# Kernel optimization log

Measured on AMD Instinct MI355X. Metric: run time of the kernel, lower is better.

Reference implementation:

```python
import jax, jax.numpy as jnp
import numpy as np

B, L, D, H = 2, 2048, 512, 8
SAMPLING_FACTOR = 5


def setup_inputs() -> dict:
    key = jax.random.key(0)
    ks = jax.random.split(key, 12)
    L_K = min(8000, L)
    log_L_K = int(np.ceil(np.log1p(L_K)))
    U_part = min(SAMPLING_FACTOR * L * log_L_K, L_K)  # = 2048
    inp = {
        'q': jax.random.normal(ks[0], (B, L, D), jnp.float32),
        'k': jax.random.normal(ks[1], (B, L, D), jnp.float32),
        'v': jax.random.normal(ks[2], (B, L, D), jnp.float32),
        'Wq': jax.random.normal(ks[3], (D, D), jnp.float32) * 0.02,
        'bq': jnp.zeros((D,), jnp.float32),
        'Wk': jax.random.normal(ks[4], (D, D), jnp.float32) * 0.02,
        'bk': jnp.zeros((D,), jnp.float32),
        'Wv': jax.random.normal(ks[5], (D, D), jnp.float32) * 0.02,
        'bv': jnp.zeros((D,), jnp.float32),
        'Wo': jax.random.normal(ks[6], (D, D), jnp.float32) * 0.02,
        'bo': jnp.zeros((D,), jnp.float32),
        'index_sample': jax.random.randint(ks[7], (U_part,), 0, L_K, jnp.int32),
    }
    return inp


def _prob_sparse(qh, Kh, Vh, index_sample):
    # qh, Kh, Vh: [B, H, L, d]
    L_K = min(8000, Kh.shape[2])  # K_sample = K[:, :8000]; L_K = its length
    L_Q = qh.shape[2]
    Ks = Kh[:, :, index_sample, :]                                  # [B,H,U,d]
    QKs = jnp.einsum('bhqd,bhkd->bhqk', qh, Ks)                     # [B,H,Lq,U]
    # M = max - sum/L_K  (source divides by L_K, not U_part)
    M = QKs.max(axis=-1) - QKs.sum(axis=-1) / L_K                   # [B,H,Lq]
    u = min(SAMPLING_FACTOR * int(np.ceil(np.log1p(L_Q))), L_Q)     # = 40
    _, M_top = jax.lax.top_k(-M, u)                                 # topk(largest=False)
    Q_red = jnp.take_along_axis(qh, M_top[..., None], axis=2)       # [B,H,u,d]
    d_k = qh.shape[-1]
    scores = jnp.einsum('bhqd,bhkd->bhqk', Q_red, Kh) / jnp.sqrt(jnp.asarray(d_k, qh.dtype))
    probs = jax.nn.softmax(scores, axis=-1)
    out = jnp.einsum('bhqk,bhkd->bhqd', probs, Vh)                  # [B,H,u,d]
    return out, scores


def reference(q, k, v, Wq, bq, Wk, bk, Wv, bv, Wo, bo, index_sample):
    qp = q @ Wq.T + bq
    kp = k @ Wk.T + bk
    vp = v @ Wv.T + bv
    Bsz, Lq, Dm = qp.shape
    d = Dm // H
    # faithful to source: q is view'd to [B,H,Lq,d] WITHOUT transpose
    qh = qp.reshape(Bsz, H, Lq, d)
    kh = kp.reshape(Bsz, -1, H, d).transpose(0, 2, 1, 3)
    vh = vp.reshape(Bsz, -1, H, d).transpose(0, 2, 1, 3)
    out, _ = _prob_sparse(qh, kh, vh, index_sample)
    u = out.shape[2]
    out = out.transpose(0, 2, 1, 3).reshape(Bsz, u, Dm)             # concat
    return out @ Wo.T + bo                                          # [B,u,D]
```

## Files before the change

### kernel.cpp

```cpp
#include <hip/hip_runtime.h>
#include <math.h>

#define B_ 2
#define L_ 2048
#define D_ 512
#define H_ 8
#define DH 64
#define NS 2048
#define NU 40
#define BHD (L_*D_)
#define QHS (L_*DH)
#define WSPM 786432

typedef __attribute__((ext_vector_type(8))) short bf16x8;
typedef __attribute__((ext_vector_type(4))) float f32x4;

__device__ inline float4 ld4(const float* p) { return *reinterpret_cast<const float4*>(p); }

__device__ inline unsigned short hi16(float x) { return (unsigned short)(__float_as_uint(x) >> 16); }
__device__ inline float trunchf(float x) { return __uint_as_float(__float_as_uint(x) & 0xFFFF0000u); }
__device__ inline void tsplit(float x, unsigned short& hs, unsigned short& ms, unsigned short& ls) {
  float h = trunchf(x); hs = hi16(x);
  float r = x - h;
  float m = trunchf(r); ms = hi16(r);
  float r2 = r - m;
  ls = hi16(r2);
}

__global__ __launch_bounds__(256) void wsplit(const float* __restrict__ Wq,
                                              const float* __restrict__ Wk,
                                              const float* __restrict__ Wv,
                                              unsigned short* __restrict__ dst,
                                              int matArg) {
  const int mat = (matArg >= 0) ? matArg : (int)blockIdx.y;
  const float* W = (mat == 0) ? Wq : (mat == 1) ? Wk : Wv;
  unsigned short* d = dst + ((matArg >= 0) ? 0 : (size_t)mat * WSPM);
  const int t = threadIdx.x;
  const int nt = blockIdx.x >> 3, g16 = blockIdx.x & 7;
  const int kc = t >> 4, lr = t & 15;
  const int n = nt*128 + g16*16 + lr;
  const float* src = W + (size_t)n*512 + kc*32;
  float xs[32];
#pragma unroll
  for (int i = 0; i < 8; ++i) {
    float4 v4 = ld4(src + 4*i);
    xs[4*i] = v4.x; xs[4*i+1] = v4.y; xs[4*i+2] = v4.z; xs[4*i+3] = v4.w;
  }
  unsigned short Hs[32], Ms[32], Ls[32];
#pragma unroll
  for (int e = 0; e < 32; ++e) tsplit(xs[e], Hs[e], Ms[e], Ls[e]);
#pragma unroll
  for (int p = 0; p < 3; ++p) {
    const unsigned short* sp = (p == 0) ? Hs : (p == 1) ? Ms : Ls;
    unsigned short* base = d + ((size_t)((p*4 + nt)*8 + g16)*16 + kc)*512;
#pragma unroll
    for (int lg = 0; lg < 4; ++lg) {
      union { bf16x8 v; unsigned short u[8]; } P;
#pragma unroll
      for (int e = 0; e < 8; ++e) P.u[e] = sp[lg*8 + e];
      *reinterpret_cast<bf16x8*>(base + (lr + 16*lg)*8) = P.v;
    }
  }
}

__global__ __launch_bounds__(256, 2) void proj_pipe(
    const float* __restrict__ qa, const float* __restrict__ ka, const float* __restrict__ va,
    const unsigned short* __restrict__ wsp,
    const float* __restrict__ bq, const float* __restrict__ bk, const float* __restrict__ bv,
    float* __restrict__ qp, float* __restrict__ kp, float* __restrict__ vp,
    int matArg)
{
  __shared__ __align__(16) unsigned short a3[2][3][128][36];
  const int t = threadIdx.x;
  const int mat = (matArg >= 0) ? matArg : (int)blockIdx.z;
  const float* A    = (mat == 0) ? qa : (mat == 1) ? ka : va;
  const float* bias = (mat == 0) ? bq : (mat == 1) ? bk : bv;
  float* C          = (mat == 0) ? qp : (mat == 1) ? kp : vp;
  const unsigned short* wspm = wsp + ((matArg >= 0) ? 0 : (size_t)mat * WSPM);
  const int m0 = blockIdx.x * 128, nt = blockIdx.y;
  const int w = t >> 6, l = t & 63;
  const int wm = w >> 1, wn = w & 1;
  const int lr = l & 15, lg = l >> 4;
  const int srow = t >> 1, sc0 = (t & 1) * 16;

  f32x4 acc[4][4];
#pragma unroll
  for (int i = 0; i < 4; ++i)
#pragma unroll
    for (int j = 0; j < 4; ++j) acc[i][j] = (f32x4){0.f, 0.f, 0.f, 0.f};

  const float* aRow = A + (size_t)(m0 + srow) * 512 + sc0;
  float4 ar0 = ld4(aRow), ar1 = ld4(aRow + 4), ar2 = ld4(aRow + 8), ar3 = ld4(aRow + 12);

  for (int kc = 0; kc < 16; ++kc) {
    const int cur = kc & 1;
    {
      float xs[16] = {ar0.x, ar0.y, ar0.z, ar0.w, ar1.x, ar1.y, ar1.z, ar1.w,
                      ar2.x, ar2.y, ar2.z, ar2.w, ar3.x, ar3.y, ar3.z, ar3.w};
#pragma unroll
      for (int hh = 0; hh < 2; ++hh) {
        union { bf16x8 v; unsigned short u[8]; } H, M, L;
#pragma unroll
        for (int e = 0; e < 8; ++e) tsplit(xs[hh*8 + e], H.u[e], M.u[e], L.u[e]);
        *reinterpret_cast<bf16x8*>(&a3[cur][0][srow][sc0 + 8*hh]) = H.v;
        *reinterpret_cast<bf16x8*>(&a3[cur][1][srow][sc0 + 8*hh]) = M.v;
        *reinterpret_cast<bf16x8*>(&a3[cur][2][srow][sc0 + 8*hh]) = L.v;
      }
    }
    bf16x8 bw[3][4];
#pragma unroll
    for (int p = 0; p < 3; ++p)
#pragma unroll
      for (int ni = 0; ni < 4; ++ni)
        bw[p][ni] = *reinterpret_cast<const bf16x8*>(
            wspm + ((size_t)((p*4 + nt)*8 + wn*4 + ni)*16 + kc)*512 + l*8);
    __syncthreads();
    if (kc < 15) {
      const float* src = A + (size_t)(m0 + srow) * 512 + (kc+1)*32 + sc0;
      ar0 = ld4(src); ar1 = ld4(src + 4); ar2 = ld4(src + 8); ar3 = ld4(src + 12);
    }
    __builtin_amdgcn_s_setprio(1);
#pragma unroll
    for (int mi = 0; mi < 4; ++mi) {
      bf16x8 a0 = *reinterpret_cast<const bf16x8*>(&a3[cur][0][wm*64 + mi*16 + lr][lg*8]);
      bf16x8 a1 = *reinterpret_cast<const bf16x8*>(&a3[cur][1][wm*64 + mi*16 + lr][lg*8]);
      bf16x8 a2 = *reinterpret_cast<const bf16x8*>(&a3[cur][2][wm*64 + mi*16 + lr][lg*8]);
#pragma unroll
      for (int ni = 0; ni < 4; ++ni) {
        acc[mi][ni] = __builtin_amdgcn_mfma_f32_16x16x32_bf16(a0, bw[0][ni], acc[mi][ni], 0, 0, 0);
        acc[mi][ni] = __builtin_amdgcn_mfma_f32_16x16x32_bf16(a0, bw[1][ni], acc[mi][ni], 0, 0, 0);
        acc[mi][ni] = __builtin_amdgcn_mfma_f32_16x16x32_bf16(a1, bw[0][ni], acc[mi][ni], 0, 0, 0);
        acc[mi][ni] = __builtin_amdgcn_mfma_f32_16x16x32_bf16(a1, bw[1][ni], acc[mi][ni], 0, 0, 0);
        acc[mi][ni] = __builtin_amdgcn_mfma_f32_16x16x32_bf16(a0, bw[2][ni], acc[mi][ni], 0, 0, 0);
        acc[mi][ni] = __builtin_amdgcn_mfma_f32_16x16x32_bf16(a2, bw[0][ni], acc[mi][ni], 0, 0, 0);
      }
    }
    __builtin_amdgcn_s_setprio(0);
  }
#pragma unroll
  for (int mi = 0; mi < 4; ++mi)
#pragma unroll
    for (int ni = 0; ni < 4; ++ni) {
      const int gn = nt*128 + wn*64 + ni*16 + lr;
      const float bv_ = bias[gn];
#pragma unroll
      for (int r = 0; r < 4; ++r) {
        const int gm = m0 + wm*64 + mi*16 + lg*4 + r;
        C[(size_t)gm * 512 + gn] = acc[mi][ni][r] + bv_;
      }
    }
}

__global__ __launch_bounds__(1024) void ksum_kernel(const float* __restrict__ kp,
                                                    const int* __restrict__ idx,
                                                    float* __restrict__ ksum) {
  __shared__ float part[16][64];
  const int bh = blockIdx.x;
  const int b = bh >> 3, h = bh & 7;
  const int t = threadIdx.x;
  const int sg = t >> 6, j = t & 63;
  const float* kbase = kp + (size_t)b*BHD + h*DH;
  float a = 0.f;
  for (int s = sg*128; s < sg*128 + 128; ++s)
    a += kbase[(size_t)idx[s]*512 + j];
  part[sg][j] = a;
  __syncthreads();
  if (t < 64) {
    float s = 0.f;
#pragma unroll
    for (int i = 0; i < 16; ++i) s += part[i][t];
    ksum[bh*64 + t] = s;
  }
}

__global__ __launch_bounds__(256, 2) void m_kernel(const float* __restrict__ qp,
                                                   const float* __restrict__ kp,
                                                   const int* __restrict__ idx,
                                                   float* __restrict__ Mp) {
  __shared__ __align__(16) unsigned short k3[3][128][72];
  const int t = threadIdx.x;
  const int bid = blockIdx.x;
  const int bh = bid >> 5, qt = (bid >> 2) & 7, ks = bid & 3;
  const int b = bh >> 3, h = bh & 7;
  const int w = t >> 6, l = t & 63;
  const int lr = l & 15;
  const int lg = l >> 4;

  bf16x8 qf[4][2][3];
  {
    const float* qbase = qp + (size_t)b*BHD + (size_t)h*QHS + (size_t)(qt*256 + w*64 + lr) * 64 + lg*8;
#pragma unroll
    for (int mi = 0; mi < 4; ++mi)
#pragma unroll
      for (int c = 0; c < 2; ++c) {
        const float* src = qbase + mi*16*64 + c*32;
        float4 x0 = ld4(src), x1 = ld4(src + 4);
        float xs[8] = {x0.x, x0.y, x0.z, x0.w, x1.x, x1.y, x1.z, x1.w};
        union { bf16x8 v; unsigned short u[8]; } H, M, L;
#pragma unroll
        for (int e = 0; e < 8; ++e) tsplit(xs[e], H.u[e], M.u[e], L.u[e]);
        qf[mi][c][0] = H.v; qf[mi][c][1] = M.v; qf[mi][c][2] = L.v;
      }
  }

  const float* kbase = kp + (size_t)b*BHD + h*DH;
  const int ib = ks * 512;
  const int srow = t >> 1, sh = (t & 1) * 32;

  float4 vst[8];
  {
    const int kr = idx[ib + srow];
    const float* src = kbase + (size_t)kr * 512 + sh;
#pragma unroll
    for (int i = 0; i < 8; ++i) vst[i] = ld4(src + 4*i);
  }

  float mx[4][4];
#pragma unroll
  for (int mi = 0; mi < 4; ++mi)
#pragma unroll
    for (int r = 0; r < 4; ++r) mx[mi][r] = -INFINITY;

  for (int tl = 0; tl < 4; ++tl) {
    __syncthreads();
    {
#pragma unroll
      for (int e2 = 0; e2 < 4; ++e2) {
        union { bf16x8 v; unsigned short u[8]; } H, M, L;
        float xs[8] = {vst[2*e2].x, vst[2*e2].y, vst[2*e2].z, vst[2*e2].w,
                       vst[2*e2+1].x, vst[2*e2+1].y, vst[2*e2+1].z, vst[2*e2+1].w};
#pragma unroll
        for (int e = 0; e < 8; ++e) tsplit(xs[e], H.u[e], M.u[e], L.u[e]);
        *reinterpret_cast<bf16x8*>(&k3[0][srow][sh + 8*e2]) = H.v;
        *reinterpret_cast<bf16x8*>(&k3[1][srow][sh + 8*e2]) = M.v;
        *reinterpret_cast<bf16x8*>(&k3[2][srow][sh + 8*e2]) = L.v;
      }
    }
    if (tl < 3) {
      const int kr = idx[ib + (tl+1)*128 + srow];
      const float* src = kbase + (size_t)kr * 512 + sh;
#pragma unroll
      for (int i = 0; i < 8; ++i) vst[i] = ld4(src + 4*i);
    }
    __syncthreads();

    for (int n2 = 0; n2 < 4; ++n2) {
      bf16x8 bf[2][3][2];
#pragma unroll
      for (int ns = 0; ns < 2; ++ns)
#pragma unroll
        for (int p = 0; p < 3; ++p)
#pragma unroll
          for (int c = 0; c < 2; ++c)
            bf[ns][p][c] = *reinterpret_cast<const bf16x8*>(&k3[p][n2*32 + ns*16 + lr][c*32 + lg*8]);
      __builtin_amdgcn_s_setprio(1);
#pragma unroll
      for (int mi = 0; mi < 4; ++mi)
#pragma unroll
        for (int ns = 0; ns < 2; ++ns) {
          f32x4 acc = {0.f, 0.f, 0.f, 0.f};
#pragma unroll
          for (int c = 0; c < 2; ++c) acc = __builtin_amdgcn_mfma_f32_16x16x32_bf16(qf[mi][c][0], bf[ns][0][c], acc, 0, 0, 0);
#pragma unroll
          for (int c = 0; c < 2; ++c) acc = __builtin_amdgcn_mfma_f32_16x16x32_bf16(qf[mi][c][0], bf[ns][1][c], acc, 0, 0, 0);
#pragma unroll
          for (int c = 0; c < 2; ++c) acc = __builtin_amdgcn_mfma_f32_16x16x32_bf16(qf[mi][c][1], bf[ns][0][c], acc, 0, 0, 0);
#pragma unroll
          for (int c = 0; c < 2; ++c) acc = __builtin_amdgcn_mfma_f32_16x16x32_bf16(qf[mi][c][1], bf[ns][1][c], acc, 0, 0, 0);
#pragma unroll
          for (int c = 0; c < 2; ++c) acc = __builtin_amdgcn_mfma_f32_16x16x32_bf16(qf[mi][c][0], bf[ns][2][c], acc, 0, 0, 0);
#pragma unroll
          for (int c = 0; c < 2; ++c) acc = __builtin_amdgcn_mfma_f32_16x16x32_bf16(qf[mi][c][2], bf[ns][0][c], acc, 0, 0, 0);
#pragma unroll
          for (int r = 0; r < 4; ++r) mx[mi][r] = fmaxf(mx[mi][r], acc[r]);
        }
      __builtin_amdgcn_s_setprio(0);
    }
  }

#pragma unroll
  for (int mi = 0; mi < 4; ++mi)
#pragma unroll
    for (int r = 0; r < 4; ++r) {
      float v = mx[mi][r];
      v = fmaxf(v, __shfl_xor(v, 1));
      v = fmaxf(v, __shfl_xor(v, 2));
      v = fmaxf(v, __shfl_xor(v, 4));
      v = fmaxf(v, __shfl_xor(v, 8));
      if (lr == 0)
        Mp[ks*32768 + bh*2048 + qt*256 + w*64 + mi*16 + lg*4 + r] = v;
    }
}

__global__ __launch_bounds__(256) void topk_kernel(const float* __restrict__ qp,
                                                   const float* __restrict__ ksum,
                                                   const float* __restrict__ Mp,
                                                   int* __restrict__ Mtop) {
  __shared__ float ks_s[64];
  __shared__ unsigned hist[256];
  __shared__ int wsum[4];
  __shared__ unsigned bitmap[64];
  __shared__ unsigned long long comb[NU];
  __shared__ int s_sel, s_rem, s_cnt;
  const int bh = blockIdx.x;
  const int b = bh >> 3, h = bh & 7;
  const int t = threadIdx.x;
  if (t < 64) ks_s[t] = ksum[bh*64 + t];
  __syncthreads();

  unsigned mykey[8];
#pragma unroll
  for (int c = 0; c < 8; ++c) {
    const int qi = c * 256 + t;
    const float* qrow = qp + (size_t)b*BHD + (size_t)h*QHS + (size_t)qi * 64;
    float dot = 0.f;
#pragma unroll
    for (int cc = 0; cc < 16; ++cc) {
      float4 q4 = ld4(qrow + 4 * cc);
      dot += q4.x * ks_s[4*cc + 0];
      dot += q4.y * ks_s[4*cc + 1];
      dot += q4.z * ks_s[4*cc + 2];
      dot += q4.w * ks_s[4*cc + 3];
    }
    const float mx2 = fmaxf(fmaxf(Mp[bh*2048 + qi], Mp[32768 + bh*2048 + qi]),
                            fmaxf(Mp[65536 + bh*2048 + qi], Mp[98304 + bh*2048 + qi]));
    const float m = mx2 - dot * (1.0f/2048.0f);
    const unsigned u = __float_as_uint(m);
    mykey[c] = (u >> 31) ? ~u : (u | 0x80000000u);
  }

  unsigned prefMask = 0u, prefVal = 0u;
  int rem = NU;
  for (int shift = 24; shift >= 0; shift -= 8) {
    hist[t] = 0;
    __syncthreads();
#pragma unroll
    for (int c = 0; c < 8; ++c) {
      const unsigned key = mykey[c];
      if ((key & prefMask) == prefVal)
        atomicAdd(&hist[(key >> shift) & 255], 1u);
    }
    __syncthreads();
    const int binc = (int)hist[t];
    int inc = binc;
#pragma unroll
    for (int off = 1; off < 64; off <<= 1) {
      const int nb = __shfl_up(inc, off);
      if ((t & 63) >= off) inc += nb;
    }
    if ((t & 63) == 63) wsum[t >> 6] = inc;
    __syncthreads();
    int wadd = 0;
    for (int w2 = 0; w2 < (t >> 6); ++w2) wadd += wsum[w2];
    const int incl = inc + wadd;
    const int excl = incl - binc;
    if (excl < rem && rem <= incl) { s_sel = t; s_rem = rem - excl; }
    __syncthreads();
    prefVal |= ((unsigned)s_sel) << shift;
    prefMask |= 0xFFu << shift;
    rem = s_rem;
    __syncthreads();
  }
  const unsigned T = prefVal;

  if (t < 64) bitmap[t] = 0;
  if (t == 0) s_cnt = 0;
  __syncthreads();
#pragma unroll
  for (int c = 0; c < 8; ++c) {
    const unsigned key = mykey[c];
    const int qi = c * 256 + t;
    if (key < T) {
      const int pos = atomicAdd(&s_cnt, 1);
      comb[pos] = ((unsigned long long)key << 11) | (unsigned)qi;
    } else if (key == T) {
      atomicOr(&bitmap[qi >> 5], 1u << (qi & 31));
    }
  }
  __syncthreads();
  if (t == 0) {
    int need = rem, cpos = s_cnt;
    for (int wd = 0; wd < 64 && need > 0; ++wd) {
      unsigned bits = bitmap[wd];
      while (bits && need > 0) {
        const int bit = __ffs(bits) - 1;
        bits &= bits - 1;
        comb[cpos++] = ((unsigned long long)T << 11) | (unsigned)(wd*32 + bit);
        --need;
      }
    }
  }
  __syncthreads();

  if (t < 64) {
    const unsigned long long mine = (t < NU) ? comb[t] : ~0ULL;
    int rank = 0;
#pragma unroll
    for (int step = 1; step < 64; ++step) {
      const unsigned long long other = __shfl(mine, (t + step) & 63);
      rank += (other < mine) ? 1 : 0;
    }
    if (t < NU) Mtop[bh*NU + rank] = (int)(mine & 0x7FFu);
  }
}

__global__ __launch_bounds__(256) void flash_partial(const float* __restrict__ qp,
                                                     const float* __restrict__ kp,
                                                     const float* __restrict__ vp,
                                                     const int* __restrict__ Mtop,
                                                     float* __restrict__ pm,
                                                     float* __restrict__ pl,
                                                     float* __restrict__ pacc) {
  __shared__ float qr[NU][65];
  __shared__ float kv[64][65];
  __shared__ float sl[NU][65];
  __shared__ float ms[NU], ls[NU], fs[NU];
  const int bid = blockIdx.x;
  const int bh = bid >> 4, kt = bid & 15;
  const int b = bh >> 3, h = bh & 7;
  const int t = threadIdx.x;
  const int g = t >> 6, j = t & 63;
  const int r4 = t >> 2, sub = t & 3;

  {
    const float* qbase = qp + (size_t)b*BHD + (size_t)h*QHS;
#pragma unroll
    for (int r = 0; r < 10; ++r) {
      const int q = g*10 + r;
      qr[q][j] = qbase[(size_t)Mtop[bh*NU + q]*64 + j];
    }
  }
  if (t < NU) { ms[t] = -INFINITY; ls[t] = 0.f; }
  float acc[10];
#pragma unroll
  for (int r = 0; r < 10; ++r) acc[r] = 0.f;

  const float* kbase = kp + (size_t)b*BHD + h*DH;
  const float* vbase = vp + (size_t)b*BHD + h*DH;
  const int srow = t >> 2, scb = (t & 3)*16;

  for (int st = 0; st < 2; ++st) {
    const int kb = kt*128 + st*64;
    __syncthreads();
    {
      const float* src = kbase + (size_t)(kb + srow)*512 + scb;
#pragma unroll
      for (int i = 0; i < 4; ++i) {
        float4 v = ld4(src + 4*i);
        kv[srow][scb + 4*i + 0] = v.x;
        kv[srow][scb + 4*i + 1] = v.y;
        kv[srow][scb + 4*i + 2] = v.z;
        kv[srow][scb + 4*i + 3] = v.w;
      }
    }
    __syncthreads();
    {
      float sv[10];
#pragma unroll
      for (int r = 0; r < 10; ++r) {
        const int q = g*10 + r;
        float s = 0.f;
#pragma unroll 8
        for (int jj = 0; jj < 64; ++jj) s += qr[q][jj]*kv[j][jj];
        sv[r] = s * 0.125f;
      }
#pragma unroll
      for (int r = 0; r < 10; ++r) sl[g*10 + r][j] = sv[r];
    }
    __syncthreads();
    float4 vst[4];
    {
      const float* src = vbase + (size_t)(kb + srow)*512 + scb;
#pragma unroll
      for (int i = 0; i < 4; ++i) vst[i] = ld4(src + 4*i);
    }
    if (r4 < NU) {
      float tm = -INFINITY;
#pragma unroll
      for (int c = 0; c < 16; ++c) tm = fmaxf(tm, sl[r4][sub*16 + c]);
      tm = fmaxf(tm, __shfl_xor(tm, 1));
      tm = fmaxf(tm, __shfl_xor(tm, 2));
      const float nm = fmaxf(ms[r4], tm);
      if (sub == 0) { fs[r4] = expf(ms[r4] - nm); ms[r4] = nm; }
    }
    __syncthreads();
    {
#pragma unroll
      for (int r = 0; r < 10; ++r) {
        const int q = g*10 + r;
        acc[r] *= fs[q];
        sl[q][j] = expf(sl[q][j] - ms[q]);
      }
#pragma unroll
      for (int i = 0; i < 4; ++i) {
        kv[srow][scb + 4*i + 0] = vst[i].x;
        kv[srow][scb + 4*i + 1] = vst[i].y;
        kv[srow][scb + 4*i + 2] = vst[i].z;
        kv[srow][scb + 4*i + 3] = vst[i].w;
      }
    }
    __syncthreads();
    if (r4 < NU) {
      float s = 0.f;
#pragma unroll
      for (int c = 0; c < 16; ++c) s += sl[r4][sub*16 + c];
      s += __shfl_xor(s, 1);
      s += __shfl_xor(s, 2);
      if (sub == 0) ls[r4] = ls[r4]*fs[r4] + s;
    }
    {
#pragma unroll 4
      for (int kk = 0; kk < 64; ++kk) {
        const float vv = kv[kk][j];
#pragma unroll
        for (int r = 0; r < 10; ++r) acc[r] += sl[g*10 + r][kk]*vv;
      }
    }
  }
  __syncthreads();
  const size_t base = (size_t)(bh*16 + kt)*NU;
  if (t < NU) { pm[base + t] = ms[t]; pl[base + t] = ls[t]; }
#pragma unroll
  for (int r = 0; r < 10; ++r)
    pacc[(base + g*10 + r)*64 + j] = acc[r];
}

__global__ __launch_bounds__(256) void flash_combine(const float* __restrict__ pm,
                                                     const float* __restrict__ pl,
                                                     const float* __restrict__ pacc,
                                                     float* __restrict__ outc) {
  const int t = threadIdx.x;
  const int qg = t >> 6, j = t & 63;
  const int bh = blockIdx.x / 10;
  const int q  = (blockIdx.x % 10)*4 + qg;
  const int b = bh >> 3, h = bh & 7;
  float m = -INFINITY;
#pragma unroll
  for (int kt = 0; kt < 16; ++kt) m = fmaxf(m, pm[(size_t)(bh*16 + kt)*NU + q]);
  float Lsum = 0.f, num = 0.f;
#pragma unroll
  for (int kt = 0; kt < 16; ++kt) {
    const size_t base = (size_t)(bh*16 + kt)*NU;
    const float w = expf(pm[base + q] - m);
    Lsum += w * pl[base + q];
    num  += w * pacc[(base + q)*64 + j];
  }
  outc[(size_t)(b*NU + q)*512 + h*64 + j] = num / Lsum;
}

__global__ __launch_bounds__(256) void wo_gemm(const float* __restrict__ outc,
                                               const float* __restrict__ Wo,
                                               float* __restrict__ pwo) {
  __shared__ __align__(16) float a_t[80][68];
  __shared__ __align__(16) float w_t[64][68];
  const int t = threadIdx.x;
  const int ty = t >> 4, tx = t & 15;
  const int nt = blockIdx.x, ks = blockIdx.y;
  float acc[5][4];
#pragma unroll
  for (int i = 0; i < 5; ++i)
#pragma unroll
    for (int j = 0; j < 4; ++j) acc[i][j] = 0.f;

  for (int c = 0; c < 2; ++c) {
    const int kb = ks*128 + c*64;
    __syncthreads();
#pragma unroll
    for (int i = 0; i < 20; ++i) {
      const int fi = t + 256*i;
      const int row = fi >> 6, col = fi & 63;
      a_t[row][col] = outc[(size_t)row*512 + kb + col];
    }
#pragma unroll
    for (int i = 0; i < 16; ++i) {
      const int fi = t + 256*i;
      const int row = fi >> 6, col = fi & 63;
      w_t[row][col] = Wo[(size_t)(nt*64 + row)*512 + kb + col];
    }
    __syncthreads();
    for (int gq = 0; gq < 16; ++gq) {
      float4 av[5], wv[4];
#pragma unroll
      for (int i = 0; i < 5; ++i) av[i] = *reinterpret_cast<const float4*>(&a_t[ty + 16*i][4*gq]);
#pragma unroll
      for (int j = 0; j < 4; ++j) wv[j] = *reinterpret_cast<const float4*>(&w_t[tx + 16*j][4*gq]);
#pragma unroll
      for (int i = 0; i < 5; ++i)
#pragma unroll
        for (int j = 0; j < 4; ++j) {
          acc[i][j] += av[i].x * wv[j].x;
          acc[i][j] += av[i].y * wv[j].y;
          acc[i][j] += av[i].z * wv[j].z;
          acc[i][j] += av[i].w * wv[j].w;
        }
    }
  }
#pragma unroll
  for (int i = 0; i < 5; ++i)
#pragma unroll
    for (int j = 0; j < 4; ++j)
      pwo[ks*40960 + (size_t)(ty + 16*i)*512 + nt*64 + tx + 16*j] = acc[i][j];
}

__global__ __launch_bounds__(256) void wo_combine(const float* __restrict__ pwo,
                                                  const float* __restrict__ bo,
                                                  float* __restrict__ out) {
  const int gi = blockIdx.x*256 + threadIdx.x;
  const float4* p = reinterpret_cast<const float4*>(pwo);
  const float4 a = p[gi], b4 = p[10240 + gi], c4 = p[20480 + gi], d4 = p[30720 + gi];
  const float4 bb = ld4(bo + 4*(gi & 127));
  float4 o;
  o.x = a.x + b4.x + c4.x + d4.x + bb.x;
  o.y = a.y + b4.y + c4.y + d4.y + bb.y;
  o.z = a.z + b4.z + c4.z + d4.z + bb.z;
  o.w = a.w + b4.w + c4.w + d4.w + bb.w;
  reinterpret_cast<float4*>(out)[gi] = o;
}

extern "C" void kernel_launch(void* const* d_in, const int* in_sizes, int n_in,
                              void* d_out, int out_size, void* d_ws, size_t ws_size,
                              hipStream_t stream) {
  const float* q  = (const float*)d_in[0];
  const float* k  = (const float*)d_in[1];
  const float* v  = (const float*)d_in[2];
  const float* Wq = (const float*)d_in[3];
  const float* bq = (const float*)d_in[4];
  const float* Wk = (const float*)d_in[5];
  const float* bk = (const float*)d_in[6];
  const float* Wv = (const float*)d_in[7];
  const float* bv = (const float*)d_in[8];
  const float* Wo = (const float*)d_in[9];
  const float* bo = (const float*)d_in[10];
  const int*  idx = (const int*)d_in[11];

  float* ws   = (float*)d_ws;
  float* qp   = ws;
  float* kp   = ws + 2097152;
  float* vp   = ws + 4194304;
  float* ksum = ws + 6291456;
  int*   Mtop = (int*)(ws + 6292480);
  float* pm   = ws + 6293120;
  float* pl   = ws + 6303360;
  float* pacc = ws + 6313600;
  float* outc = ws + 6968960;
  float* Mp   = pm;
  float* pwo  = pm;
  unsigned short* wsp = (unsigned short*)(ws + 6291456);

  const dim3 blk(256);
  const bool bigws = (ws_size >= (size_t)7471104 * 4);
  if (bigws) {
    wsplit<<<dim3(32, 3), blk, 0, stream>>>(Wq, Wk, Wv, wsp, -1);
    proj_pipe<<<dim3(32, 4, 3), blk, 0, stream>>>(q, k, v, wsp, bq, bk, bv, qp, kp, vp, -1);
  } else {
    for (int m = 0; m < 3; ++m) {
      wsplit<<<dim3(32, 1), blk, 0, stream>>>(Wq, Wk, Wv, wsp, m);
      proj_pipe<<<dim3(32, 4, 1), blk, 0, stream>>>(q, k, v, wsp, bq, bk, bv, qp, kp, vp, m);
    }
  }
  ksum_kernel<<<dim3(16), dim3(1024), 0, stream>>>(kp, idx, ksum);
  m_kernel<<<dim3(512), blk, 0, stream>>>(qp, kp, idx, Mp);
  topk_kernel<<<dim3(16), blk, 0, stream>>>(qp, ksum, Mp, Mtop);
  flash_partial<<<dim3(256), blk, 0, stream>>>(qp, kp, vp, Mtop, pm, pl, pacc);
  flash_combine<<<dim3(160), blk, 0, stream>>>(pm, pl, pacc, outc);
  wo_gemm<<<dim3(8, 4), blk, 0, stream>>>(outc, Wo, pwo);
  wo_combine<<<dim3(40), blk, 0, stream>>>(pwo, bo, (float*)d_out);
}
```

Measured before the change: 189.8 us.

## Deduplicate sampled key indices for the max pass and double-buffer projection weights

A new single-block kernel builds a bitmap of the sampled key indices and compacts it into a sorted unique list, padded to whole 128-row tiles. The max-score kernel then loops only over the unique tiles, since duplicates cannot change a max, and splits the key range 8 ways instead of 4 to keep the larger grid busy. The row sum still uses the full index list, so duplicates are still counted there. Separately, the projection GEMM is unrolled by two with ping-pong registers so the next step's weight fragments and input rows are prefetched before the current MFMA block runs. Costs: an extra launch, a serial single-block dedupe, more partial-max buffers for top-k to read, and higher register pressure in the projection.

```diff
diff --git a/kernel.cpp b/kernel.cpp
--- a/kernel.cpp
+++ b/kernel.cpp
@@ -82,6 +82,7 @@
   const int wm = w >> 1, wn = w & 1;
   const int lr = l & 15, lg = l >> 4;
   const int srow = t >> 1, sc0 = (t & 1) * 16;
+  const float* aRow = A + (size_t)(m0 + srow) * 512 + sc0;
 
   f32x4 acc[4][4];
 #pragma unroll
@@ -89,54 +90,75 @@
 #pragma unroll
     for (int j = 0; j < 4; ++j) acc[i][j] = (f32x4){0.f, 0.f, 0.f, 0.f};
 
-  const float* aRow = A + (size_t)(m0 + srow) * 512 + sc0;
-  float4 ar0 = ld4(aRow), ar1 = ld4(aRow + 4), ar2 = ld4(aRow + 8), ar3 = ld4(aRow + 12);
-
-  for (int kc = 0; kc < 16; ++kc) {
-    const int cur = kc & 1;
-    {
-      float xs[16] = {ar0.x, ar0.y, ar0.z, ar0.w, ar1.x, ar1.y, ar1.z, ar1.w,
-                      ar2.x, ar2.y, ar2.z, ar2.w, ar3.x, ar3.y, ar3.z, ar3.w};
-#pragma unroll
-      for (int hh = 0; hh < 2; ++hh) {
-        union { bf16x8 v; unsigned short u[8]; } H, M, L;
-#pragma unroll
-        for (int e = 0; e < 8; ++e) tsplit(xs[hh*8 + e], H.u[e], M.u[e], L.u[e]);
-        *reinterpret_cast<bf16x8*>(&a3[cur][0][srow][sc0 + 8*hh]) = H.v;
-        *reinterpret_cast<bf16x8*>(&a3[cur][1][srow][sc0 + 8*hh]) = M.v;
-        *reinterpret_cast<bf16x8*>(&a3[cur][2][srow][sc0 + 8*hh]) = L.v;
-      }
-    }
-    bf16x8 bw[3][4];
-#pragma unroll
-    for (int p = 0; p < 3; ++p)
-#pragma unroll
-      for (int ni = 0; ni < 4; ++ni)
-        bw[p][ni] = *reinterpret_cast<const bf16x8*>(
-            wspm + ((size_t)((p*4 + nt)*8 + wn*4 + ni)*16 + kc)*512 + l*8);
+#define LOADW(dst, kcv)                                                        \
+  _Pragma("unroll")                                                            \
+  for (int p = 0; p < 3; ++p)                                                  \
+    _Pragma("unroll")                                                          \
+    for (int ni = 0; ni < 4; ++ni)                                             \
+      dst[p][ni] = *reinterpret_cast<const bf16x8*>(                           \
+          wspm + ((size_t)((p*4 + nt)*8 + wn*4 + ni)*16 + (kcv))*512 + l*8);
+
+#define SPLITSTORE(r0, r1, r2, r3, buf)                                        \
+  {                                                                            \
+    float xs[16] = {r0.x, r0.y, r0.z, r0.w, r1.x, r1.y, r1.z, r1.w,            \
+                    r2.x, r2.y, r2.z, r2.w, r3.x, r3.y, r3.z, r3.w};           \
+    _Pragma("unroll")                                                          \
+    for (int hh = 0; hh < 2; ++hh) {                                           \
+      union { bf16x8 v; unsigned short u[8]; } H, M, L;                        \
+      _Pragma("unroll")                                                        \
+      for (int e = 0; e < 8; ++e) tsplit(xs[hh*8 + e], H.u[e], M.u[e], L.u[e]);\
+      *reinterpret_cast<bf16x8*>(&a3[buf][0][srow][sc0 + 8*hh]) = H.v;         \
+      *reinterpret_cast<bf16x8*>(&a3[buf][1][srow][sc0 + 8*hh]) = M.v;         \
+      *reinterpret_cast<bf16x8*>(&a3[buf][2][srow][sc0 + 8*hh]) = L.v;         \
+    }                                                                          \
+  }
+
+#define MFMA6(buf, bw)                                                         \
+  __builtin_amdgcn_s_setprio(1);                                               \
+  _Pragma("unroll")                                                            \
+  for (int mi = 0; mi < 4; ++mi) {                                             \
+    bf16x8 a0 = *reinterpret_cast<const bf16x8*>(&a3[buf][0][wm*64 + mi*16 + lr][lg*8]); \
+    bf16x8 a1 = *reinterpret_cast<const bf16x8*>(&a3[buf][1][wm*64 + mi*16 + lr][lg*8]); \
+    bf16x8 a2 = *reinterpret_cast<const bf16x8*>(&a3[buf][2][wm*64 + mi*16 + lr][lg*8]); \
+    _Pragma("unroll")                                                          \
+    for (int ni = 0; ni < 4; ++ni) {                                           \
+      acc[mi][ni] = __builtin_amdgcn_mfma_f32_16x16x32_bf16(a0, bw[0][ni], acc[mi][ni], 0, 0, 0); \
+      acc[mi][ni] = __builtin_amdgcn_mfma_f32_16x16x32_bf16(a0, bw[1][ni], acc[mi][ni], 0, 0, 0); \
+      acc[mi][ni] = __builtin_amdgcn_mfma_f32_16x16x32_bf16(a1, bw[0][ni], acc[mi][ni], 0, 0, 0); \
+      acc[mi][ni] = __builtin_amdgcn_mfma_f32_16x16x32_bf16(a1, bw[1][ni], acc[mi][ni], 0, 0, 0); \
+      acc[mi][ni] = __builtin_amdgcn_mfma_f32_16x16x32_bf16(a0, bw[2][ni], acc[mi][ni], 0, 0, 0); \
+      acc[mi][ni] = __builtin_amdgcn_mfma_f32_16x16x32_bf16(a2, bw[0][ni], acc[mi][ni], 0, 0, 0); \
+    }                                                                          \
+  }                                                                            \
+  __builtin_amdgcn_s_setprio(0);
+
+  float4 arA0 = ld4(aRow), arA1 = ld4(aRow + 4), arA2 = ld4(aRow + 8), arA3 = ld4(aRow + 12);
+  bf16x8 bwA[3][4], bwB[3][4];
+  LOADW(bwA, 0);
+  float4 arB0, arB1, arB2, arB3;
+
+  for (int kc = 0; kc < 16; kc += 2) {
+    SPLITSTORE(arA0, arA1, arA2, arA3, 0);
     __syncthreads();
     if (kc < 15) {
-      const float* src = A + (size_t)(m0 + srow) * 512 + (kc+1)*32 + sc0;
-      ar0 = ld4(src); ar1 = ld4(src + 4); ar2 = ld4(src + 8); ar3 = ld4(src + 12);
-    }
-    __builtin_amdgcn_s_setprio(1);
-#pragma unroll
-    for (int mi = 0; mi < 4; ++mi) {
-      bf16x8 a0 = *reinterpret_cast<const bf16x8*>(&a3[cur][0][wm*64 + mi*16 + lr][lg*8]);
-      bf16x8 a1 = *reinterpret_cast<const bf16x8*>(&a3[cur][1][wm*64 + mi*16 + lr][lg*8]);
-      bf16x8 a2 = *reinterpret_cast<const bf16x8*>(&a3[cur][2][wm*64 + mi*16 + lr][lg*8]);
-#pragma unroll
-      for (int ni = 0; ni < 4; ++ni) {
-        acc[mi][ni] = __builtin_amdgcn_mfma_f32_16x16x32_bf16(a0, bw[0][ni], acc[mi][ni], 0, 0, 0);
-        acc[mi][ni] = __builtin_amdgcn_mfma_f32_16x16x32_bf16(a0, bw[1][ni], acc[mi][ni], 0, 0, 0);
-        acc[mi][ni] = __builtin_amdgcn_mfma_f32_16x16x32_bf16(a1, bw[0][ni], acc[mi][ni], 0, 0, 0);
-        acc[mi][ni] = __builtin_amdgcn_mfma_f32_16x16x32_bf16(a1, bw[1][ni], acc[mi][ni], 0, 0, 0);
-        acc[mi][ni] = __builtin_amdgcn_mfma_f32_16x16x32_bf16(a0, bw[2][ni], acc[mi][ni], 0, 0, 0);
-        acc[mi][ni] = __builtin_amdgcn_mfma_f32_16x16x32_bf16(a2, bw[0][ni], acc[mi][ni], 0, 0, 0);
-      }
-    }
-    __builtin_amdgcn_s_setprio(0);
-  }
+      const float* src = aRow + (kc+1)*32;
+      arB0 = ld4(src); arB1 = ld4(src + 4); arB2 = ld4(src + 8); arB3 = ld4(src + 12);
+      LOADW(bwB, kc+1);
+    }
+    MFMA6(0, bwA);
+    SPLITSTORE(arB0, arB1, arB2, arB3, 1);
+    __syncthreads();
+    if (kc + 2 < 16) {
+      const float* src = aRow + (kc+2)*32;
+      arA0 = ld4(src); arA1 = ld4(src + 4); arA2 = ld4(src + 8); arA3 = ld4(src + 12);
+      LOADW(bwA, kc+2);
+    }
+    MFMA6(1, bwB);
+  }
+#undef LOADW
+#undef SPLITSTORE
+#undef MFMA6
+
 #pragma unroll
   for (int mi = 0; mi < 4; ++mi)
 #pragma unroll
@@ -173,14 +195,60 @@
   }
 }
 
+__global__ __launch_bounds__(256) void dedupe(const int* __restrict__ idx,
+                                              int* __restrict__ ulist,
+                                              int* __restrict__ ucnt) {
+  __shared__ unsigned bm[64];
+  __shared__ int base[64];
+  __shared__ int total;
+  const int t = threadIdx.x;
+  if (t < 64) bm[t] = 0;
+  __syncthreads();
+#pragma unroll
+  for (int c = 0; c < 8; ++c) {
+    const int v = idx[c*256 + t];
+    atomicOr(&bm[v >> 5], 1u << (v & 31));
+  }
+  __syncthreads();
+  if (t < 64) {
+    const int cnt = __popc(bm[t]);
+    int inc = cnt;
+#pragma unroll
+    for (int off = 1; off < 64; off <<= 1) {
+      const int nb = __shfl_up(inc, off);
+      if (t >= off) inc += nb;
+    }
+    base[t] = inc - cnt;
+    if (t == 63) total = inc;
+  }
+  __syncthreads();
+  if (t < 64) {
+    unsigned w = bm[t];
+    int pos = base[t];
+    while (w) {
+      const int b = __ffs(w) - 1;
+      w &= w - 1;
+      ulist[pos++] = t*32 + b;
+    }
+  }
+  __syncthreads();
+  const int U = total;
+  const int nt = (U + 127) >> 7;
+  const int padded = nt << 7;
+  const int first = ulist[0];
+  for (int p = U + t; p < padded; p += 256) ulist[p] = first;
+  if (t == 0) ucnt[0] = nt;
+}
+
 __global__ __launch_bounds__(256, 2) void m_kernel(const float* __restrict__ qp,
                                                    const float* __restrict__ kp,
-                                                   const int* __restrict__ idx,
+                                                   const int* __restrict__ ulist,
+                                                   const int* __restrict__ ucnt,
                                                    float* __restrict__ Mp) {
   __shared__ __align__(16) unsigned short k3[3][128][72];
   const int t = threadIdx.x;
   const int bid = blockIdx.x;
-  const int bh = bid >> 5, qt = (bid >> 2) & 7, ks = bid & 3;
+  const int bh = bid >> 6, qt = (bid >> 3) & 7, ks = bid & 7;
   const int b = bh >> 3, h = bh & 7;
   const int w = t >> 6, l = t & 63;
   const int lr = l & 15;
@@ -204,12 +272,12 @@
   }
 
   const float* kbase = kp + (size_t)b*BHD + h*DH;
-  const int ib = ks * 512;
+  const int ntiles = ucnt[0];
   const int srow = t >> 1, sh = (t & 1) * 32;
 
   float4 vst[8];
-  {
-    const int kr = idx[ib + srow];
+  if (ks < ntiles) {
+    const int kr = ulist[ks*128 + srow];
     const float* src = kbase + (size_t)kr * 512 + sh;
 #pragma unroll
     for (int i = 0; i < 8; ++i) vst[i] = ld4(src + 4*i);
@@ -221,7 +289,7 @@
 #pragma unroll
     for (int r = 0; r < 4; ++r) mx[mi][r] = -INFINITY;
 
-  for (int tl = 0; tl < 4; ++tl) {
+  for (int ti = ks; ti < ntiles; ti += 8) {
     __syncthreads();
     {
 #pragma unroll
@@ -236,8 +304,8 @@
         *reinterpret_cast<bf16x8*>(&k3[2][srow][sh + 8*e2]) = L.v;
       }
     }
-    if (tl < 3) {
-      const int kr = idx[ib + (tl+1)*128 + srow];
+    if (ti + 8 < ntiles) {
+      const int kr = ulist[(ti+8)*128 + srow];
       const float* src = kbase + (size_t)kr * 512 + sh;
 #pragma unroll
       for (int i = 0; i < 8; ++i) vst[i] = ld4(src + 4*i);
@@ -322,9 +390,10 @@
       dot += q4.z * ks_s[4*cc + 2];
       dot += q4.w * ks_s[4*cc + 3];
     }
-    const float mx2 = fmaxf(fmaxf(Mp[bh*2048 + qi], Mp[32768 + bh*2048 + qi]),
-                            fmaxf(Mp[65536 + bh*2048 + qi], Mp[98304 + bh*2048 + qi]));
-    const float m = mx2 - dot * (1.0f/2048.0f);
+    float mxv = Mp[bh*2048 + qi];
+#pragma unroll
+    for (int s = 1; s < 8; ++s) mxv = fmaxf(mxv, Mp[s*32768 + bh*2048 + qi]);
+    const float m = mxv - dot * (1.0f/2048.0f);
     const unsigned u = __float_as_uint(m);
     mykey[c] = (u >> 31) ? ~u : (u | 0x80000000u);
   }
@@ -646,6 +715,8 @@
   float* Mp   = pm;
   float* pwo  = pm;
   unsigned short* wsp = (unsigned short*)(ws + 6291456);
+  int* ulist = (int*)(ws + 6600000);
+  int* ucnt  = ulist + 2048;
 
   const dim3 blk(256);
   const bool bigws = (ws_size >= (size_t)7471104 * 4);
@@ -659,7 +730,8 @@
     }
   }
   ksum_kernel<<<dim3(16), dim3(1024), 0, stream>>>(kp, idx, ksum);
-  m_kernel<<<dim3(512), blk, 0, stream>>>(qp, kp, idx, Mp);
+  dedupe<<<dim3(1), blk, 0, stream>>>(idx, ulist, ucnt);
+  m_kernel<<<dim3(1024), blk, 0, stream>>>(qp, kp, ulist, ucnt, Mp);
   topk_kernel<<<dim3(16), blk, 0, stream>>>(qp, ksum, Mp, Mtop);
   flash_partial<<<dim3(256), blk, 0, stream>>>(qp, kp, vp, Mtop, pm, pl, pacc);
   flash_combine<<<dim3(160), blk, 0, stream>>>(pm, pl, pacc, outc);
```

After: 201.2 us. +6.0%, slower.
